# Performance work log

Measured on AMD Instinct MI355X. Metric: run time of the kernel, lower is better.

Reference implementation:

```python
import jax, jax.numpy as jnp
import numpy as np

B, N, D2H, U = 16, 1024, 1024, 512  # batch of sentences, tokens, 2*lstm_dims, hidden_units


def setup_inputs() -> dict:
    key = jax.random.key(0)
    ks = jax.random.split(key, 7)
    s = 1.0 / np.sqrt(D2H)
    return {
        "x": jax.random.normal(ks[0], (B, N, D2H), dtype=jnp.float32),
        "W_h": jax.random.normal(ks[1], (U, D2H), dtype=jnp.float32) * s,
        "b_h": jax.random.normal(ks[2], (U,), dtype=jnp.float32) * 0.01,
        "W_m": jax.random.normal(ks[3], (U, D2H), dtype=jnp.float32) * s,
        "b_m": jax.random.normal(ks[4], (U,), dtype=jnp.float32) * 0.01,
        "w_out": jax.random.normal(ks[5], (U,), dtype=jnp.float32) * (1.0 / np.sqrt(U)),
        "b_out": jax.random.normal(ks[6], (), dtype=jnp.float32) * 0.01,
    }


def reference(x, W_h, b_h, W_m, b_m, w_out, b_out):
    # headfov[i] = W_h @ x_i + b_h ; modfov[j] = W_m @ x_j + b_m
    H = jnp.einsum("bnd,ud->bnu", x, W_h) + b_h  # [B, N, U]
    M = jnp.einsum("bnd,ud->bnu", x, W_m) + b_m  # [B, N, U]
    # score[i,j] = w_out . (H_i + M_j) + b_out  (outLayer is linear, so it
    # distributes over the add; avoids materializing an [B,N,N,U] tensor)
    sH = jnp.einsum("bnu,u->bn", H, w_out)  # [B, N]
    sM = jnp.einsum("bnu,u->bn", M, w_out)  # [B, N]
    scores = sH[:, :, None] + sM[:, None, :] + b_out  # [B, N, N]
    return scores
```

## Files before the change

### kernel.cpp

```cpp
#include <hip/hip_runtime.h>

#define BB 16
#define NN 1024
#define DD 1024
#define UU 512

__global__ __launch_bounds__(256) void prep_kernel(
    const float* __restrict__ W_h, const float* __restrict__ W_m,
    const float* __restrict__ b_h, const float* __restrict__ b_m,
    const float* __restrict__ w_out, const float* __restrict__ b_out,
    float* __restrict__ v_h, float* __restrict__ v_m, float* __restrict__ Cc) {
    int t = threadIdx.x;
    int blk = blockIdx.x;
    if (blk < 128) {
        const float* W = (blk < 64) ? W_h : W_m;
        float* v = (blk < 64) ? v_h : v_m;
        int b = blk & 63;
        int d = (b & 3) * 256 + t;
        int u0 = (b >> 2) * 32;
        float acc = 0.f;
        #pragma unroll
        for (int k = 0; k < 32; ++k) {
            acc += W[(size_t)(u0 + k) * DD + d] * w_out[u0 + k];
        }
        atomicAdd(v + d, acc);
    } else {
        __shared__ float red[256];
        float acc = 0.f;
        for (int u = t; u < UU; u += 256) acc += (b_h[u] + b_m[u]) * w_out[u];
        red[t] = acc;
        __syncthreads();
        for (int s = 128; s > 0; s >>= 1) {
            if (t < s) red[t] += red[t + s];
            __syncthreads();
        }
        if (t == 0) *Cc = red[0] + b_out[0];
    }
}

__global__ __launch_bounds__(256) void row_dots_kernel(
    const float* __restrict__ x,
    const float* __restrict__ v_h, const float* __restrict__ v_m,
    const float* __restrict__ Cc,
    float* __restrict__ sH, float* __restrict__ sM) {
    int t = threadIdx.x;
    int wave = t >> 6, lane = t & 63;
    int row = blockIdx.x * 4 + wave;
    const float4* xr = (const float4*)(x + (size_t)row * DD);
    const float4* vh = (const float4*)v_h;
    const float4* vm = (const float4*)v_m;

    float ah = 0.f, am = 0.f;
    #pragma unroll
    for (int k = 0; k < 4; ++k) {
        int idx = lane + 64 * k;
        float4 xv = xr[idx];
        float4 hv = vh[idx];
        float4 mv = vm[idx];
        ah += xv.x * hv.x + xv.y * hv.y + xv.z * hv.z + xv.w * hv.w;
        am += xv.x * mv.x + xv.y * mv.y + xv.z * mv.z + xv.w * mv.w;
    }
    #pragma unroll
    for (int off = 32; off > 0; off >>= 1) {
        ah += __shfl_down(ah, off, 64);
        am += __shfl_down(am, off, 64);
    }
    if (lane == 0) {
        sH[row] = ah + *Cc;
        sM[row] = am;
    }
}

__global__ __launch_bounds__(256) void scores_kernel(
    const float* __restrict__ sH, const float* __restrict__ sM,
    float4* __restrict__ out) {
    int bi = blockIdx.x;
    int j4 = threadIdx.x;
    float h = sH[bi];
    const float4* mrow = (const float4*)(sM + (bi & ~(NN - 1)));
    float4 m = mrow[j4];
    float4 o;
    o.x = h + m.x;
    o.y = h + m.y;
    o.z = h + m.z;
    o.w = h + m.w;
    out[(size_t)bi * (NN / 4) + j4] = o;
}

extern "C" void kernel_launch(void* const* d_in, const int* in_sizes, int n_in,
                              void* d_out, int out_size, void* d_ws, size_t ws_size,
                              hipStream_t stream) {
    const float* x     = (const float*)d_in[0];
    const float* W_h   = (const float*)d_in[1];
    const float* b_h   = (const float*)d_in[2];
    const float* W_m   = (const float*)d_in[3];
    const float* b_m   = (const float*)d_in[4];
    const float* w_out = (const float*)d_in[5];
    const float* b_out = (const float*)d_in[6];
    float* out = (float*)d_out;

    float* ws  = (float*)d_ws;
    float* v_h = ws;
    float* v_m = ws + 1024;
    float* Cc  = ws + 2048;
    float* sH  = ws + 4096;
    float* sM  = ws + 4096 + 16384;

    hipMemsetAsync(ws, 0, 2048 * sizeof(float), stream);

    prep_kernel<<<129, 256, 0, stream>>>(W_h, W_m, b_h, b_m, w_out, b_out, v_h, v_m, Cc);
    row_dots_kernel<<<BB * NN / 4, 256, 0, stream>>>(x, v_h, v_m, Cc, sH, sM);
    scores_kernel<<<BB * NN, 256, 0, stream>>>(sH, sM, (float4*)out);
}
```

Before: 127.6 us.

## Fuse prep, row-dot and score kernels into one cooperative grid-synced kernel

After: 199.0 us. 1.56x slower.

```diff
diff --git a/kernel.cpp b/kernel.cpp
--- a/kernel.cpp
+++ b/kernel.cpp
@@ -1,90 +1,104 @@
 #include <hip/hip_runtime.h>
+#include <hip/hip_cooperative_groups.h>
+
+namespace cg = cooperative_groups;
 
 #define BB 16
 #define NN 1024
 #define DD 1024
 #define UU 512
 
-__global__ __launch_bounds__(256) void prep_kernel(
-    const float* __restrict__ W_h, const float* __restrict__ W_m,
-    const float* __restrict__ b_h, const float* __restrict__ b_m,
+__global__ __launch_bounds__(1024, 4) void fused_kernel(
+    const float* __restrict__ x,
+    const float* __restrict__ W_h, const float* __restrict__ b_h,
+    const float* __restrict__ W_m, const float* __restrict__ b_m,
     const float* __restrict__ w_out, const float* __restrict__ b_out,
-    float* __restrict__ v_h, float* __restrict__ v_m, float* __restrict__ Cc) {
-    int t = threadIdx.x;
-    int blk = blockIdx.x;
-    if (blk < 128) {
-        const float* W = (blk < 64) ? W_h : W_m;
-        float* v = (blk < 64) ? v_h : v_m;
-        int b = blk & 63;
-        int d = (b & 3) * 256 + t;
-        int u0 = (b >> 2) * 32;
+    float* __restrict__ v,
+    float* __restrict__ Cc,
+    float* __restrict__ sH,
+    float* __restrict__ sM,
+    float* __restrict__ out) {
+    cg::grid_group grid = cg::this_grid();
+    const int t = threadIdx.x;
+    const int blk = blockIdx.x;
+
+    __shared__ float red[8][128];
+    if (blk < 16) {
+        const int m = blk >> 3;
+        const int d0 = (blk & 7) * 128;
+        const float* W = m ? W_m : W_h;
+        const int dl = t & 127;
+        const int p = t >> 7;
+        const float* Wp = W + (size_t)(p * 64) * DD + d0 + dl;
         float acc = 0.f;
         #pragma unroll
-        for (int k = 0; k < 32; ++k) {
-            acc += W[(size_t)(u0 + k) * DD + d] * w_out[u0 + k];
+        for (int k = 0; k < 64; ++k)
+            acc += Wp[(size_t)k * DD] * w_out[p * 64 + k];
+        red[p][dl] = acc;
+        __syncthreads();
+        if (t < 128) {
+            float s = 0.f;
+            #pragma unroll
+            for (int q = 0; q < 8; ++q) s += red[q][t];
+            v[m * DD + d0 + t] = s;
         }
-        atomicAdd(v + d, acc);
-    } else {
-        __shared__ float red[256];
+    } else if (blk == 16) {
+        __shared__ float r2[512];
         float acc = 0.f;
-        for (int u = t; u < UU; u += 256) acc += (b_h[u] + b_m[u]) * w_out[u];
-        red[t] = acc;
+        if (t < UU) acc = (b_h[t] + b_m[t]) * w_out[t];
+        if (t < 512) r2[t] = acc;
         __syncthreads();
-        for (int s = 128; s > 0; s >>= 1) {
-            if (t < s) red[t] += red[t + s];
+        for (int s = 256; s > 0; s >>= 1) {
+            if (t < s) r2[t] += r2[t + s];
             __syncthreads();
         }
-        if (t == 0) *Cc = red[0] + b_out[0];
+        if (t == 0) *Cc = r2[0] + b_out[0];
     }
-}
+    grid.sync();
 
-__global__ __launch_bounds__(256) void row_dots_kernel(
-    const float* __restrict__ x,
-    const float* __restrict__ v_h, const float* __restrict__ v_m,
-    const float* __restrict__ Cc,
-    float* __restrict__ sH, float* __restrict__ sM) {
-    int t = threadIdx.x;
-    int wave = t >> 6, lane = t & 63;
-    int row = blockIdx.x * 4 + wave;
-    const float4* xr = (const float4*)(x + (size_t)row * DD);
-    const float4* vh = (const float4*)v_h;
-    const float4* vm = (const float4*)v_m;
+    {
+        const float C = *Cc;
+        const int lane = t & 63;
+        const int gwave = blk * 16 + (t >> 6);
+        const float4* vh = (const float4*)v;
+        const float4* vm = (const float4*)(v + DD);
+        for (int r = gwave; r < BB * NN; r += 4096) {
+            const float4* xr = (const float4*)(x + (size_t)r * DD);
+            float ah = 0.f, am = 0.f;
+            #pragma unroll
+            for (int k = 0; k < 4; ++k) {
+                int idx = lane + 64 * k;
+                float4 xv = xr[idx];
+                float4 hv = vh[idx];
+                float4 mv = vm[idx];
+                ah += xv.x*hv.x + xv.y*hv.y + xv.z*hv.z + xv.w*hv.w;
+                am += xv.x*mv.x + xv.y*mv.y + xv.z*mv.z + xv.w*mv.w;
+            }
+            #pragma unroll
+            for (int off = 32; off > 0; off >>= 1) {
+                ah += __shfl_down(ah, off, 64);
+                am += __shfl_down(am, off, 64);
+            }
+            if (lane == 0) { sH[r] = ah + C; sM[r] = am; }
+        }
+    }
+    grid.sync();
 
-    float ah = 0.f, am = 0.f;
-    #pragma unroll
-    for (int k = 0; k < 4; ++k) {
-        int idx = lane + 64 * k;
-        float4 xv = xr[idx];
-        float4 hv = vh[idx];
-        float4 mv = vm[idx];
-        ah += xv.x * hv.x + xv.y * hv.y + xv.z * hv.z + xv.w * hv.w;
-        am += xv.x * mv.x + xv.y * mv.y + xv.z * mv.z + xv.w * mv.w;
+    {
+        const int bi0 = blk * 64;
+        const int b = bi0 >> 10;
+        const int j4 = t & 255;
+        const int rsub = t >> 8;
+        const float4 mv = ((const float4*)(sM + b * NN))[j4];
+        float4* out4 = (float4*)out;
+        #pragma unroll
+        for (int it = 0; it < 16; ++it) {
+            int bi = bi0 + rsub + 4 * it;
+            float h = sH[bi];
+            float4 o = { h + mv.x, h + mv.y, h + mv.z, h + mv.w };
+            out4[(size_t)bi * 256 + j4] = o;
+        }
     }
-    #pragma unroll
-    for (int off = 32; off > 0; off >>= 1) {
-        ah += __shfl_down(ah, off, 64);
-        am += __shfl_down(am, off, 64);
-    }
-    if (lane == 0) {
-        sH[row] = ah + *Cc;
-        sM[row] = am;
-    }
-}
-
-__global__ __launch_bounds__(256) void scores_kernel(
-    const float* __restrict__ sH, const float* __restrict__ sM,
-    float4* __restrict__ out) {
-    int bi = blockIdx.x;
-    int j4 = threadIdx.x;
-    float h = sH[bi];
-    const float4* mrow = (const float4*)(sM + (bi & ~(NN - 1)));
-    float4 m = mrow[j4];
-    float4 o;
-    o.x = h + m.x;
-    o.y = h + m.y;
-    o.z = h + m.z;
-    o.w = h + m.w;
-    out[(size_t)bi * (NN / 4) + j4] = o;
 }
 
 extern "C" void kernel_launch(void* const* d_in, const int* in_sizes, int n_in,
@@ -99,16 +113,14 @@
     const float* b_out = (const float*)d_in[6];
     float* out = (float*)d_out;
 
-    float* ws  = (float*)d_ws;
-    float* v_h = ws;
-    float* v_m = ws + 1024;
-    float* Cc  = ws + 2048;
-    float* sH  = ws + 4096;
-    float* sM  = ws + 4096 + 16384;
+    float* ws = (float*)d_ws;
+    float* v  = ws;
+    float* Cc = ws + 2048;
+    float* sH = ws + 4096;
+    float* sM = ws + 4096 + 16384;
 
-    hipMemsetAsync(ws, 0, 2048 * sizeof(float), stream);
-
-    prep_kernel<<<129, 256, 0, stream>>>(W_h, W_m, b_h, b_m, w_out, b_out, v_h, v_m, Cc);
-    row_dots_kernel<<<BB * NN / 4, 256, 0, stream>>>(x, v_h, v_m, Cc, sH, sM);
-    scores_kernel<<<BB * NN, 256, 0, stream>>>(sH, sM, (float4*)out);
+    void* args[] = {(void*)&x, (void*)&W_h, (void*)&b_h, (void*)&W_m, (void*)&b_m,
+                    (void*)&w_out, (void*)&b_out, (void*)&v, (void*)&Cc,
+                    (void*)&sH, (void*)&sM, (void*)&out};
+    hipLaunchCooperativeKernel((void*)fused_kernel, dim3(256), dim3(1024), args, 0, stream);
 }
```
